# Kernel optimization log

Measured on AMD Instinct MI355X. Metric: run time of the kernel, lower is better.

The kernel has to match this reference:

```python
import jax, jax.numpy as jnp
from jax import lax
import numpy as np

N, D = 1024, 100000
K, SELECT_N = 20, 256  # select_n = int(N * split) = int(1024 * 0.25)


def setup_inputs() -> dict:
    key = jax.random.key(0)
    k1, k2 = jax.random.split(key)
    inp = jax.random.normal(k1, (N, D), dtype=jnp.float32)
    indices = jax.random.randint(k2, (K, SELECT_N), 0, N, dtype=jnp.int32)
    return {"inp": inp, "indices": indices}


def reference(inp, indices):
    # For each of k bagging rounds: gather select_n random rows, max over rows.
    # scan over k keeps the peak intermediate at [select_n, D] instead of [k, select_n, D].
    def step(_, idx):
        return None, jnp.max(inp[idx], axis=0)  # [D]

    _, maxes = lax.scan(step, None, indices)   # [k, D]
    return jnp.mean(maxes, axis=0, keepdims=True)  # [1, D]
```

## Files before the change

kernel.cpp:

```cpp
#include <hip/hip_runtime.h>


#define N_ROWS   1024
#define D_COLS   100000
#define K_ROUNDS 20
#define SEL_N    256
#define NIDX     (K_ROUNDS * SEL_N)
#define VEC      2
#define CPB      (64 * VEC)
#define BLOCK    256
#define WAVES    4
#define RPW      (N_ROWS / WAVES)
#define CHUNK    4
#define NEG_INF  (-3.402823466e+38f)

__device__ __forceinline__ void load_chunk(float2 (&v)[CHUNK], unsigned int (&m)[CHUNK],
                                           const float* __restrict__ p,
                                           const unsigned int* smask,
                                           int r0, int base) {
    #pragma unroll
    for (int j = 0; j < CHUNK; ++j) {
        v[j] = *reinterpret_cast<const float2*>(p + (size_t)(r0 + base + j) * D_COLS);
        m[j] = smask[r0 + base + j];
    }
}

__device__ __forceinline__ void process_chunk(const float2 (&v)[CHUNK],
                                              const unsigned int (&mm)[CHUNK],
                                              float2 (&acc)[K_ROUNDS]) {
    const unsigned int s0 = (unsigned int)__builtin_amdgcn_readfirstlane((int)mm[0]);
    const unsigned int s1 = (unsigned int)__builtin_amdgcn_readfirstlane((int)mm[1]);
    const unsigned int s2 = (unsigned int)__builtin_amdgcn_readfirstlane((int)mm[2]);
    const unsigned int s3 = (unsigned int)__builtin_amdgcn_readfirstlane((int)mm[3]);
    #pragma unroll
    for (int k = 0; k < K_ROUNDS; ++k) {
        const unsigned int bit = 1u << k;
        const float a0x = (s0 & bit) ? v[0].x : NEG_INF;
        const float a0y = (s0 & bit) ? v[0].y : NEG_INF;
        const float a1x = (s1 & bit) ? v[1].x : NEG_INF;
        const float a1y = (s1 & bit) ? v[1].y : NEG_INF;
        const float a2x = (s2 & bit) ? v[2].x : NEG_INF;
        const float a2y = (s2 & bit) ? v[2].y : NEG_INF;
        const float a3x = (s3 & bit) ? v[3].x : NEG_INF;
        const float a3y = (s3 & bit) ? v[3].y : NEG_INF;
        acc[k].x = fmaxf(fmaxf(acc[k].x, a0x), a1x);
        acc[k].y = fmaxf(fmaxf(acc[k].y, a0y), a1y);
        acc[k].x = fmaxf(fmaxf(acc[k].x, a2x), a3x);
        acc[k].y = fmaxf(fmaxf(acc[k].y, a2y), a3y);
    }
}

__global__ __launch_bounds__(BLOCK, 4) void bagmax_kernel(
    const float* __restrict__ inp,
    const int*   __restrict__ indices,
    float*       __restrict__ out)
{
    __shared__ unsigned int smask[N_ROWS];
    __shared__ float2 part[WAVES - 1][K_ROUNDS][64];

    const int tid  = threadIdx.x;
    const int lane = tid & 63;
    const int wave = tid >> 6;

    for (int i = tid; i < N_ROWS; i += BLOCK) smask[i] = 0u;
    __syncthreads();
    for (int i = tid; i < NIDX; i += BLOCK) {
        atomicOr(&smask[indices[i]], 1u << (i >> 8));
    }
    __syncthreads();

    const int colbase = blockIdx.x * CPB + lane * VEC;
    const int colc    = colbase <= D_COLS - VEC ? colbase : D_COLS - VEC;
    const float* p    = inp + colc;
    const int r0      = wave * RPW;

    float2 acc[K_ROUNDS];
    #pragma unroll
    for (int k = 0; k < K_ROUNDS; ++k) acc[k] = make_float2(NEG_INF, NEG_INF);

    float2 A[CHUNK], B[CHUNK];
    unsigned int mA[CHUNK], mB[CHUNK];
    load_chunk(A, mA, p, smask, r0, 0);
    #pragma unroll 1
    for (int c = 0; c < RPW; c += 2 * CHUNK) {
        load_chunk(B, mB, p, smask, r0, c + CHUNK);
        process_chunk(A, mA, acc);
        const int nb = (c + 2 * CHUNK <= RPW - CHUNK) ? (c + 2 * CHUNK) : (RPW - CHUNK);
        load_chunk(A, mA, p, smask, r0, nb);
        process_chunk(B, mB, acc);
    }

    if (wave > 0) {
        #pragma unroll
        for (int k = 0; k < K_ROUNDS; ++k) part[wave - 1][k][lane] = acc[k];
    }
    __syncthreads();
    if (wave == 0) {
        float sx = 0.f, sy = 0.f;
        #pragma unroll
        for (int k = 0; k < K_ROUNDS; ++k) {
            const float2 p0 = part[0][k][lane];
            const float2 p1 = part[1][k][lane];
            const float2 p2 = part[2][k][lane];
            sx += fmaxf(fmaxf(acc[k].x, p0.x), fmaxf(p1.x, p2.x));
            sy += fmaxf(fmaxf(acc[k].y, p0.y), fmaxf(p1.y, p2.y));
        }
        if (colbase <= D_COLS - VEC) {
            *reinterpret_cast<float2*>(out + colbase) =
                make_float2(sx * (1.0f / K_ROUNDS), sy * (1.0f / K_ROUNDS));
        }
    }
}

extern "C" void kernel_launch(void* const* d_in, const int* in_sizes, int n_in,
                              void* d_out, int out_size, void* d_ws, size_t ws_size,
                              hipStream_t stream) {
    const float* inp     = (const float*)d_in[0];
    const int*   indices = (const int*)d_in[1];
    float*       out     = (float*)d_out;

    const int grid = (D_COLS + CPB - 1) / CPB;
    bagmax_kernel<<<grid, BLOCK, 0, stream>>>(inp, indices, out);
}
```

Measured before the change: 137.8 us.

## Split row reduction across two blocks and combine partial maxima in second kernel

Splits the 1024-row reduction across two blocks per column tile (grid y dimension), so twice as many blocks are launched. Each block writes per-round partial maxima to workspace, and a second kernel takes the max of the two halves and averages over rounds. The aim is more parallelism and occupancy for the bandwidth-bound pass. The cost is a second launch plus about 16 MB of workspace written and then read back, and every block still rebuilds the full row mask.

```diff
diff --git a/kernel.cpp b/kernel.cpp
--- a/kernel.cpp
+++ b/kernel.cpp
@@ -10,9 +10,12 @@
 #define CPB      (64 * VEC)
 #define BLOCK    256
 #define WAVES    4
-#define RPW      (N_ROWS / WAVES)
+#define ROWSPLIT 2
+#define RPB      (N_ROWS / ROWSPLIT)
+#define RPW      (RPB / WAVES)
 #define CHUNK    4
 #define NEG_INF  (-3.402823466e+38f)
+#define NCB      ((D_COLS + CPB - 1) / CPB)
 
 __device__ __forceinline__ void load_chunk(float2 (&v)[CHUNK], unsigned int (&m)[CHUNK],
                                            const float* __restrict__ p,
@@ -50,10 +53,10 @@
     }
 }
 
-__global__ __launch_bounds__(BLOCK, 4) void bagmax_kernel(
+__global__ __launch_bounds__(BLOCK, 4) void bagmax_part_kernel(
     const float* __restrict__ inp,
     const int*   __restrict__ indices,
-    float*       __restrict__ out)
+    float*       __restrict__ ws)
 {
     __shared__ unsigned int smask[N_ROWS];
     __shared__ float2 part[WAVES - 1][K_ROUNDS][64];
@@ -61,6 +64,7 @@
     const int tid  = threadIdx.x;
     const int lane = tid & 63;
     const int wave = tid >> 6;
+    const int rs   = blockIdx.y;
 
     for (int i = tid; i < N_ROWS; i += BLOCK) smask[i] = 0u;
     __syncthreads();
@@ -72,7 +76,7 @@
     const int colbase = blockIdx.x * CPB + lane * VEC;
     const int colc    = colbase <= D_COLS - VEC ? colbase : D_COLS - VEC;
     const float* p    = inp + colc;
-    const int r0      = wave * RPW;
+    const int r0      = rs * RPB + wave * RPW;
 
     float2 acc[K_ROUNDS];
     #pragma unroll
@@ -95,21 +99,38 @@
         for (int k = 0; k < K_ROUNDS; ++k) part[wave - 1][k][lane] = acc[k];
     }
     __syncthreads();
-    if (wave == 0) {
-        float sx = 0.f, sy = 0.f;
+    if (wave == 0 && colbase <= D_COLS - VEC) {
         #pragma unroll
         for (int k = 0; k < K_ROUNDS; ++k) {
             const float2 p0 = part[0][k][lane];
             const float2 p1 = part[1][k][lane];
             const float2 p2 = part[2][k][lane];
-            sx += fmaxf(fmaxf(acc[k].x, p0.x), fmaxf(p1.x, p2.x));
-            sy += fmaxf(fmaxf(acc[k].y, p0.y), fmaxf(p1.y, p2.y));
-        }
-        if (colbase <= D_COLS - VEC) {
-            *reinterpret_cast<float2*>(out + colbase) =
-                make_float2(sx * (1.0f / K_ROUNDS), sy * (1.0f / K_ROUNDS));
+            float2 m;
+            m.x = fmaxf(fmaxf(acc[k].x, p0.x), fmaxf(p1.x, p2.x));
+            m.y = fmaxf(fmaxf(acc[k].y, p0.y), fmaxf(p1.y, p2.y));
+            *reinterpret_cast<float2*>(ws + ((size_t)(rs * K_ROUNDS + k)) * D_COLS + colbase) = m;
         }
     }
+}
+
+__global__ __launch_bounds__(BLOCK) void bagmax_final_kernel(
+    const float* __restrict__ ws,
+    float*       __restrict__ out)
+{
+    const int t = blockIdx.x * BLOCK + threadIdx.x;
+    const int col = t * VEC;
+    if (col > D_COLS - VEC) return;
+
+    float sx = 0.f, sy = 0.f;
+    #pragma unroll
+    for (int k = 0; k < K_ROUNDS; ++k) {
+        const float2 w0 = *reinterpret_cast<const float2*>(ws + ((size_t)(0 * K_ROUNDS + k)) * D_COLS + col);
+        const float2 w1 = *reinterpret_cast<const float2*>(ws + ((size_t)(1 * K_ROUNDS + k)) * D_COLS + col);
+        sx += fmaxf(w0.x, w1.x);
+        sy += fmaxf(w0.y, w1.y);
+    }
+    *reinterpret_cast<float2*>(out + col) =
+        make_float2(sx * (1.0f / K_ROUNDS), sy * (1.0f / K_ROUNDS));
 }
 
 extern "C" void kernel_launch(void* const* d_in, const int* in_sizes, int n_in,
@@ -118,7 +139,12 @@
     const float* inp     = (const float*)d_in[0];
     const int*   indices = (const int*)d_in[1];
     float*       out     = (float*)d_out;
+    float*       ws      = (float*)d_ws;
 
-    const int grid = (D_COLS + CPB - 1) / CPB;
-    bagmax_kernel<<<grid, BLOCK, 0, stream>>>(inp, indices, out);
+    dim3 grid1(NCB, ROWSPLIT);
+    bagmax_part_kernel<<<grid1, BLOCK, 0, stream>>>(inp, indices, ws);
+
+    const int nthr2 = D_COLS / VEC;
+    const int grid2 = (nthr2 + BLOCK - 1) / BLOCK;
+    bagmax_final_kernel<<<grid2, BLOCK, 0, stream>>>(ws, out);
 }
```

Result: slower. 270.3 us (+96.1%).
